# Kernel tuning notes

Hardware: AMD Instinct MI355X
Metric: run time of the kernel (lower is better)

## Reference

```python
import jax, jax.numpy as jnp
import numpy as np

N, DIN, DOUT = 8192, 256, 128
NEG_SLOPE = 0.01         # F.leaky_relu default
MASK_VAL = -9.0e15       # from the torch source


def setup_inputs() -> dict:
    key = jax.random.key(0)
    kx, kadj, kW, kbW, ka1, ka2, kba = jax.random.split(key, 7)
    x = jax.random.normal(kx, (N, DIN), dtype=jnp.float32)
    adj = jax.random.randint(kadj, (N, N), 0, 2, dtype=jnp.int32)
    # Linear W: input_dim -> output_dim
    W = jax.random.normal(kW, (DIN, DOUT), dtype=jnp.float32) * (1.0 / np.sqrt(DIN))
    bW = jax.random.normal(kbW, (DOUT,), dtype=jnp.float32) * 0.01
    # Linear a: 2*output_dim -> 1, split into the h_i part (a1) and h_j part (a2)
    a1 = jax.random.normal(ka1, (DOUT,), dtype=jnp.float32) * (1.0 / np.sqrt(2 * DOUT))
    a2 = jax.random.normal(ka2, (DOUT,), dtype=jnp.float32) * (1.0 / np.sqrt(2 * DOUT))
    ba = jax.random.normal(kba, (), dtype=jnp.float32) * 0.01
    return {"x": x, "adj": adj, "W": W, "bW": bW, "a1": a1, "a2": a2, "ba": ba}


def reference(x, adj, W, bW, a1, a2, ba):
    # h = W x + b  -> [N, DOUT]
    h = x @ W + bW
    # e[i,j] = leaky_relu(a . [h_i, h_j] + ba) = leaky_relu(a1.h_i + a2.h_j + ba)
    s_src = h @ a1            # [N]
    s_dst = h @ a2            # [N]
    e = s_src[:, None] + s_dst[None, :] + ba   # [N, N]
    e = jnp.where(e > 0, e, NEG_SLOPE * e)
    # mask non-edges, row softmax over neighbors j
    e = jnp.where(adj > 0, e, MASK_VAL)
    alpha = jax.nn.softmax(e, axis=1)          # [N, N]
    # dropout is identity in eval mode (dropout_rate=0)
    return alpha @ h                            # [N, DOUT]
```

## Files before the change

### kernel.cpp

```cpp
#include <hip/hip_runtime.h>
#include <hip/hip_bf16.h>


#define NN 8192
#define DIN 256
#define DOUT 128
#define LOG2E 1.4426950408889634f

typedef __attribute__((ext_vector_type(8))) short short8;
typedef __attribute__((ext_vector_type(4))) float floatx4;

__global__ void prep_wt(const float* __restrict__ W, __hip_bfloat16* __restrict__ WT) {
    int e = blockIdx.x * blockDim.x + threadIdx.x;
    if (e < DIN * DOUT) {
        int k = e >> 7;
        int d = e & 127;
        WT[d * DIN + k] = __float2bfloat16(W[e]);
    }
}

__global__ __launch_bounds__(256, 4) void gat_h(
    const float* __restrict__ x, const __hip_bfloat16* __restrict__ WT,
    const float* __restrict__ bW, const float* __restrict__ a1, const float* __restrict__ a2,
    __hip_bfloat16* __restrict__ hbB, float* __restrict__ s_src, float* __restrict__ s_dst) {
    int tid = threadIdx.x;
    int w = tid >> 6, lane = tid & 63;
    int lm = lane & 15, lq = lane >> 4;
    int i0 = blockIdx.x * 32;
    int r0 = (w >> 1) * 16;
    int c0 = (w & 1) * 64;

    __shared__ float s1s[32], s2s[32];
    if (tid < 32) { s1s[tid] = 0.f; s2s[tid] = 0.f; }
    __syncthreads();

    floatx4 acc[4] = {};
#pragma unroll
    for (int kk = 0; kk < DIN; kk += 32) {
        const float4* xp = (const float4*)&x[(size_t)(i0 + r0 + lm) * DIN + kk + lq * 8];
        float4 xa = xp[0], xb = xp[1];
        union { short8 v; __hip_bfloat16 h[8]; } af;
        af.h[0] = __float2bfloat16(xa.x); af.h[1] = __float2bfloat16(xa.y);
        af.h[2] = __float2bfloat16(xa.z); af.h[3] = __float2bfloat16(xa.w);
        af.h[4] = __float2bfloat16(xb.x); af.h[5] = __float2bfloat16(xb.y);
        af.h[6] = __float2bfloat16(xb.z); af.h[7] = __float2bfloat16(xb.w);
#pragma unroll
        for (int t = 0; t < 4; t++) {
            int d = c0 + 16 * t + lm;
            short8 bf = *(const short8*)&WT[(size_t)d * DIN + kk + lq * 8];
            acc[t] = __builtin_amdgcn_mfma_f32_16x16x32_bf16(af.v, bf, acc[t], 0, 0, 0);
        }
    }
    float s1[4] = {0.f, 0.f, 0.f, 0.f}, s2[4] = {0.f, 0.f, 0.f, 0.f};
#pragma unroll
    for (int t = 0; t < 4; t++) {
        int d = c0 + 16 * t + lm;
        int f = (c0 >> 4) + t;
        float A1 = a1[d], A2 = a2[d], B = bW[d];
#pragma unroll
        for (int r = 0; r < 4; r++) {
            int k = r0 + lq * 4 + r;
            float h = acc[t][r] + B;
            hbB[(size_t)blockIdx.x * 4096 + f * 512 + (k >> 3) * 128 + lm * 8 + (k & 7)] =
                __float2bfloat16(h);
            s1[r] += h * A1;
            s2[r] += h * A2;
        }
    }
#pragma unroll
    for (int r = 0; r < 4; r++) {
        for (int m = 1; m < 16; m <<= 1) {
            s1[r] += __shfl_xor(s1[r], m, 64);
            s2[r] += __shfl_xor(s2[r], m, 64);
        }
    }
    if (lm == 0) {
#pragma unroll
        for (int r = 0; r < 4; r++) {
            int row = r0 + lq * 4 + r;
            atomicAdd(&s1s[row], s1[r]);
            atomicAdd(&s2s[row], s2[r]);
        }
    }
    __syncthreads();
    if (tid < 32) {
        s_src[i0 + tid] = s1s[tid] * LOG2E;
        s_dst[i0 + tid] = s2s[tid] * LOG2E;
    }
}

template <int NJT>
__global__ void build_mask(const int* __restrict__ adj, unsigned char* __restrict__ mask) {
    size_t gid = (size_t)blockIdx.x * blockDim.x + threadIdx.x;
    const int4* a = (const int4*)(adj + gid * 8);
    int4 v0 = a[0], v1 = a[1];
    unsigned int b = 0;
    b |= (v0.x != 0) ? 1u : 0u;
    b |= (v0.y != 0) ? 2u : 0u;
    b |= (v0.z != 0) ? 4u : 0u;
    b |= (v0.w != 0) ? 8u : 0u;
    b |= (v1.x != 0) ? 16u : 0u;
    b |= (v1.y != 0) ? 32u : 0u;
    b |= (v1.z != 0) ? 64u : 0u;
    b |= (v1.w != 0) ? 128u : 0u;
    unsigned int g = (unsigned int)gid & (NJT * 4 - 1);
    size_t pos = (gid & ~(size_t)(NJT * 4 - 1)) | ((g & 3) * NJT + (g >> 2));
    mask[pos] = (unsigned char)b;
}

__device__ inline short8 make_pfrag(unsigned int cm, float ssi, float4 cd0, float4 cd1,
                                    floatx4* accd, const short8 ones) {
    float p[8];
    float e;
    e = ssi + cd0.x; e = fmaxf(e, 0.01f * e); p[0] = (cm & 1u)   ? __builtin_amdgcn_exp2f(e) : 0.f;
    e = ssi + cd0.y; e = fmaxf(e, 0.01f * e); p[1] = (cm & 2u)   ? __builtin_amdgcn_exp2f(e) : 0.f;
    e = ssi + cd0.z; e = fmaxf(e, 0.01f * e); p[2] = (cm & 4u)   ? __builtin_amdgcn_exp2f(e) : 0.f;
    e = ssi + cd0.w; e = fmaxf(e, 0.01f * e); p[3] = (cm & 8u)   ? __builtin_amdgcn_exp2f(e) : 0.f;
    e = ssi + cd1.x; e = fmaxf(e, 0.01f * e); p[4] = (cm & 16u)  ? __builtin_amdgcn_exp2f(e) : 0.f;
    e = ssi + cd1.y; e = fmaxf(e, 0.01f * e); p[5] = (cm & 32u)  ? __builtin_amdgcn_exp2f(e) : 0.f;
    e = ssi + cd1.z; e = fmaxf(e, 0.01f * e); p[6] = (cm & 64u)  ? __builtin_amdgcn_exp2f(e) : 0.f;
    e = ssi + cd1.w; e = fmaxf(e, 0.01f * e); p[7] = (cm & 128u) ? __builtin_amdgcn_exp2f(e) : 0.f;
    union { short8 v; __hip_bfloat162 q[4]; } af;
    af.q[0] = __float22bfloat162_rn(make_float2(p[0], p[1]));
    af.q[1] = __float22bfloat162_rn(make_float2(p[2], p[3]));
    af.q[2] = __float22bfloat162_rn(make_float2(p[4], p[5]));
    af.q[3] = __float22bfloat162_rn(make_float2(p[6], p[7]));
    *accd = __builtin_amdgcn_mfma_f32_16x16x32_bf16(af.v, ones, *accd, 0, 0, 0);
    return af.v;
}

template <int NJT>
__global__ __launch_bounds__(256, 3) void gat_attn(
    const unsigned char* __restrict__ mask, const float* __restrict__ s_src,
    const float* __restrict__ s_dst, const float* __restrict__ ba_p,
    const __hip_bfloat16* __restrict__ hbB,
    float* __restrict__ num, float* __restrict__ lpart) {
    int tid = threadIdx.x;
    int w = tid >> 6, lane = tid & 63;
    int lm = lane & 15, lq = lane >> 4;
    int b = blockIdx.x;
    int ib = b & 63;
    int jh = b >> 6;
    int i0 = ib * 128 + w * 32;
    int jb0 = jh * (NJT * 32);

    const unsigned char* mrow0 = mask + (size_t)(i0 + lm) * (NN / 8) + jh * (NJT * 4) + lq * NJT;
    const unsigned char* mrow1 = mrow0 + (size_t)16 * (NN / 8);
    union Mr { uint4 v[NJT / 16]; unsigned int u[NJT / 4]; };
    Mr mr0, mr1;
#pragma unroll
    for (int q = 0; q < NJT / 16; q++) {
        mr0.v[q] = ((const uint4*)mrow0)[q];
        mr1.v[q] = ((const uint4*)mrow1)[q];
    }

    float ba = ba_p[0] * LOG2E;
    float ssi0 = s_src[i0 + lm] + ba;
    float ssi1 = s_src[i0 + 16 + lm] + ba;
    const float* sd = s_dst + jb0 + lq * 8;
    const __hip_bfloat16* hb = hbB + ((size_t)(jh * NJT) * 8) * 512 + lane * 8;

    floatx4 acc0[8] = {}, acc1[8] = {};
    floatx4 accd0 = {}, accd1 = {};
    const short8 ones = { 0x3F80, 0x3F80, 0x3F80, 0x3F80, 0x3F80, 0x3F80, 0x3F80, 0x3F80 };

#pragma unroll
    for (int t = 0; t < NJT; t++) {
        unsigned int cm0 = (mr0.u[t >> 2] >> ((t & 3) * 8)) & 0xFFu;
        unsigned int cm1 = (mr1.u[t >> 2] >> ((t & 3) * 8)) & 0xFFu;
        float4 cd0 = *(const float4*)(sd + t * 32);
        float4 cd1 = *(const float4*)(sd + t * 32 + 4);
        short8 af0 = make_pfrag(cm0, ssi0, cd0, cd1, &accd0, ones);
        short8 af1 = make_pfrag(cm1, ssi1, cd0, cd1, &accd1, ones);

        const __hip_bfloat16* hbt = hb + (size_t)t * 8 * 512;
#pragma unroll
        for (int f = 0; f < 8; f++) {
            short8 bf = *(const short8*)(hbt + f * 512);
            acc0[f] = __builtin_amdgcn_mfma_f32_16x16x32_bf16(af0, bf, acc0[f], 0, 0, 0);
            acc1[f] = __builtin_amdgcn_mfma_f32_16x16x32_bf16(af1, bf, acc1[f], 0, 0, 0);
        }
    }

    float* nb = num + ((size_t)jh * NN + i0) * DOUT;
#pragma unroll
    for (int f = 0; f < 8; f++)
#pragma unroll
        for (int r = 0; r < 4; r++) {
            nb[(size_t)(lq * 4 + r) * DOUT + f * 16 + lm] = acc0[f][r];
            nb[(size_t)(16 + lq * 4 + r) * DOUT + f * 16 + lm] = acc1[f][r];
        }
    if (lm == 0) {
#pragma unroll
        for (int r = 0; r < 4; r++) {
            lpart[(size_t)jh * NN + i0 + lq * 4 + r] = accd0[r];
            lpart[(size_t)jh * NN + i0 + 16 + lq * 4 + r] = accd1[r];
        }
    }
}

__global__ void gat_combine(const float* __restrict__ num, const float* __restrict__ lpart,
                            float* __restrict__ out, int jsplit) {
    int gid = blockIdx.x * blockDim.x + threadIdx.x;
    int idx = gid * 4;
    int i = idx >> 7;
    float den = 0.f;
    for (int s = 0; s < jsplit; s++) den += lpart[(size_t)s * NN + i];
    float inv = 1.0f / den;
    float4 o = make_float4(0.f, 0.f, 0.f, 0.f);
    for (int s = 0; s < jsplit; s++) {
        float4 n = *(const float4*)&num[(size_t)s * NN * DOUT + idx];
        o.x += n.x; o.y += n.y; o.z += n.z; o.w += n.w;
    }
    o.x *= inv; o.y *= inv; o.z *= inv; o.w *= inv;
    *(float4*)&out[idx] = o;
}

extern "C" void kernel_launch(void* const* d_in, const int* in_sizes, int n_in,
                              void* d_out, int out_size, void* d_ws, size_t ws_size,
                              hipStream_t stream) {
    const float* x  = (const float*)d_in[0];
    const int* adj  = (const int*)d_in[1];
    const float* W  = (const float*)d_in[2];
    const float* bW = (const float*)d_in[3];
    const float* a1 = (const float*)d_in[4];
    const float* a2 = (const float*)d_in[5];
    const float* ba = (const float*)d_in[6];
    float* out = (float*)d_out;

    char* ws = (char*)d_ws;
    __hip_bfloat16* hbB  = (__hip_bfloat16*)ws;
    __hip_bfloat16* WT   = (__hip_bfloat16*)(ws + 2097152);
    float* s_src         = (float*)(ws + 2162688);
    float* s_dst         = (float*)(ws + 2195456);
    float* lpart         = (float*)(ws + 2228224);
    unsigned char* mask  = (unsigned char*)(ws + 2752512);
    float* num           = (float*)(ws + 11141120);

    int jsplit = (ws_size >= 11141120 + (size_t)16 * NN * DOUT * 4) ? 16 : 8;

    if (jsplit == 16) build_mask<16><<<32768, 256, 0, stream>>>(adj, mask);
    else              build_mask<32><<<32768, 256, 0, stream>>>(adj, mask);
    prep_wt<<<128, 256, 0, stream>>>(W, WT);
    gat_h<<<256, 256, 0, stream>>>(x, WT, bW, a1, a2, hbB, s_src, s_dst);
    if (jsplit == 16)
        gat_attn<16><<<1024, 256, 0, stream>>>(mask, s_src, s_dst, ba, hbB, num, lpart);
    else
        gat_attn<32><<<512, 256, 0, stream>>>(mask, s_src, s_dst, ba, hbB, num, lpart);
    gat_combine<<<1024, 256, 0, stream>>>(num, lpart, out, jsplit);
}
```

Measured before the change: 440.1 us.

## Fuse adjacency mask building into attention kernel and use nontemporal memory ops

Removes the separate bitmask-packing kernel and has the attention kernel load int32 adjacency values directly with nontemporal loads, testing nonzero per element. This eliminates one full pass over the adjacency matrix plus the packed mask write/read. The attention kernel now streams far more bytes itself, so it may become bandwidth-limited if latency is not hidden. Partial-sum stores and combine loads are also marked nontemporal to reduce cache pollution.

```diff
diff --git a/kernel.cpp b/kernel.cpp
--- a/kernel.cpp
+++ b/kernel.cpp
@@ -9,6 +9,7 @@
 
 typedef __attribute__((ext_vector_type(8))) short short8;
 typedef __attribute__((ext_vector_type(4))) float floatx4;
+typedef __attribute__((ext_vector_type(4))) unsigned int uintx4;
 
 __global__ void prep_wt(const float* __restrict__ W, __hip_bfloat16* __restrict__ WT) {
     int e = blockIdx.x * blockDim.x + threadIdx.x;
@@ -89,37 +90,18 @@
     }
 }
 
-template <int NJT>
-__global__ void build_mask(const int* __restrict__ adj, unsigned char* __restrict__ mask) {
-    size_t gid = (size_t)blockIdx.x * blockDim.x + threadIdx.x;
-    const int4* a = (const int4*)(adj + gid * 8);
-    int4 v0 = a[0], v1 = a[1];
-    unsigned int b = 0;
-    b |= (v0.x != 0) ? 1u : 0u;
-    b |= (v0.y != 0) ? 2u : 0u;
-    b |= (v0.z != 0) ? 4u : 0u;
-    b |= (v0.w != 0) ? 8u : 0u;
-    b |= (v1.x != 0) ? 16u : 0u;
-    b |= (v1.y != 0) ? 32u : 0u;
-    b |= (v1.z != 0) ? 64u : 0u;
-    b |= (v1.w != 0) ? 128u : 0u;
-    unsigned int g = (unsigned int)gid & (NJT * 4 - 1);
-    size_t pos = (gid & ~(size_t)(NJT * 4 - 1)) | ((g & 3) * NJT + (g >> 2));
-    mask[pos] = (unsigned char)b;
-}
-
-__device__ inline short8 make_pfrag(unsigned int cm, float ssi, float4 cd0, float4 cd1,
+__device__ inline short8 make_pfrag(uintx4 m0, uintx4 m1, float ssi, float4 cd0, float4 cd1,
                                     floatx4* accd, const short8 ones) {
     float p[8];
     float e;
-    e = ssi + cd0.x; e = fmaxf(e, 0.01f * e); p[0] = (cm & 1u)   ? __builtin_amdgcn_exp2f(e) : 0.f;
-    e = ssi + cd0.y; e = fmaxf(e, 0.01f * e); p[1] = (cm & 2u)   ? __builtin_amdgcn_exp2f(e) : 0.f;
-    e = ssi + cd0.z; e = fmaxf(e, 0.01f * e); p[2] = (cm & 4u)   ? __builtin_amdgcn_exp2f(e) : 0.f;
-    e = ssi + cd0.w; e = fmaxf(e, 0.01f * e); p[3] = (cm & 8u)   ? __builtin_amdgcn_exp2f(e) : 0.f;
-    e = ssi + cd1.x; e = fmaxf(e, 0.01f * e); p[4] = (cm & 16u)  ? __builtin_amdgcn_exp2f(e) : 0.f;
-    e = ssi + cd1.y; e = fmaxf(e, 0.01f * e); p[5] = (cm & 32u)  ? __builtin_amdgcn_exp2f(e) : 0.f;
-    e = ssi + cd1.z; e = fmaxf(e, 0.01f * e); p[6] = (cm & 64u)  ? __builtin_amdgcn_exp2f(e) : 0.f;
-    e = ssi + cd1.w; e = fmaxf(e, 0.01f * e); p[7] = (cm & 128u) ? __builtin_amdgcn_exp2f(e) : 0.f;
+    e = ssi + cd0.x; e = fmaxf(e, 0.01f * e); p[0] = m0.x ? __builtin_amdgcn_exp2f(e) : 0.f;
+    e = ssi + cd0.y; e = fmaxf(e, 0.01f * e); p[1] = m0.y ? __builtin_amdgcn_exp2f(e) : 0.f;
+    e = ssi + cd0.z; e = fmaxf(e, 0.01f * e); p[2] = m0.z ? __builtin_amdgcn_exp2f(e) : 0.f;
+    e = ssi + cd0.w; e = fmaxf(e, 0.01f * e); p[3] = m0.w ? __builtin_amdgcn_exp2f(e) : 0.f;
+    e = ssi + cd1.x; e = fmaxf(e, 0.01f * e); p[4] = m1.x ? __builtin_amdgcn_exp2f(e) : 0.f;
+    e = ssi + cd1.y; e = fmaxf(e, 0.01f * e); p[5] = m1.y ? __builtin_amdgcn_exp2f(e) : 0.f;
+    e = ssi + cd1.z; e = fmaxf(e, 0.01f * e); p[6] = m1.z ? __builtin_amdgcn_exp2f(e) : 0.f;
+    e = ssi + cd1.w; e = fmaxf(e, 0.01f * e); p[7] = m1.w ? __builtin_amdgcn_exp2f(e) : 0.f;
     union { short8 v; __hip_bfloat162 q[4]; } af;
     af.q[0] = __float22bfloat162_rn(make_float2(p[0], p[1]));
     af.q[1] = __float22bfloat162_rn(make_float2(p[2], p[3]));
@@ -131,7 +113,7 @@
 
 template <int NJT>
 __global__ __launch_bounds__(256, 3) void gat_attn(
-    const unsigned char* __restrict__ mask, const float* __restrict__ s_src,
+    const int* __restrict__ adj, const float* __restrict__ s_src,
     const float* __restrict__ s_dst, const float* __restrict__ ba_p,
     const __hip_bfloat16* __restrict__ hbB,
     float* __restrict__ num, float* __restrict__ lpart) {
@@ -144,15 +126,8 @@
     int i0 = ib * 128 + w * 32;
     int jb0 = jh * (NJT * 32);
 
-    const unsigned char* mrow0 = mask + (size_t)(i0 + lm) * (NN / 8) + jh * (NJT * 4) + lq * NJT;
-    const unsigned char* mrow1 = mrow0 + (size_t)16 * (NN / 8);
-    union Mr { uint4 v[NJT / 16]; unsigned int u[NJT / 4]; };
-    Mr mr0, mr1;
-#pragma unroll
-    for (int q = 0; q < NJT / 16; q++) {
-        mr0.v[q] = ((const uint4*)mrow0)[q];
-        mr1.v[q] = ((const uint4*)mrow1)[q];
-    }
+    const int* arow0 = adj + (size_t)(i0 + lm) * NN + jb0 + lq * 8;
+    const int* arow1 = arow0 + (size_t)16 * NN;
 
     float ba = ba_p[0] * LOG2E;
     float ssi0 = s_src[i0 + lm] + ba;
@@ -166,12 +141,16 @@
 
 #pragma unroll
     for (int t = 0; t < NJT; t++) {
-        unsigned int cm0 = (mr0.u[t >> 2] >> ((t & 3) * 8)) & 0xFFu;
-        unsigned int cm1 = (mr1.u[t >> 2] >> ((t & 3) * 8)) & 0xFFu;
+        const uintx4* a0p = (const uintx4*)(arow0 + t * 32);
+        const uintx4* a1p = (const uintx4*)(arow1 + t * 32);
+        uintx4 m00 = __builtin_nontemporal_load(a0p);
+        uintx4 m01 = __builtin_nontemporal_load(a0p + 1);
+        uintx4 m10 = __builtin_nontemporal_load(a1p);
+        uintx4 m11 = __builtin_nontemporal_load(a1p + 1);
         float4 cd0 = *(const float4*)(sd + t * 32);
         float4 cd1 = *(const float4*)(sd + t * 32 + 4);
-        short8 af0 = make_pfrag(cm0, ssi0, cd0, cd1, &accd0, ones);
-        short8 af1 = make_pfrag(cm1, ssi1, cd0, cd1, &accd1, ones);
+        short8 af0 = make_pfrag(m00, m01, ssi0, cd0, cd1, &accd0, ones);
+        short8 af1 = make_pfrag(m10, m11, ssi1, cd0, cd1, &accd1, ones);
 
         const __hip_bfloat16* hbt = hb + (size_t)t * 8 * 512;
 #pragma unroll
@@ -187,8 +166,10 @@
     for (int f = 0; f < 8; f++)
 #pragma unroll
         for (int r = 0; r < 4; r++) {
-            nb[(size_t)(lq * 4 + r) * DOUT + f * 16 + lm] = acc0[f][r];
-            nb[(size_t)(16 + lq * 4 + r) * DOUT + f * 16 + lm] = acc1[f][r];
+            __builtin_nontemporal_store(acc0[f][r],
+                &nb[(size_t)(lq * 4 + r) * DOUT + f * 16 + lm]);
+            __builtin_nontemporal_store(acc1[f][r],
+                &nb[(size_t)(16 + lq * 4 + r) * DOUT + f * 16 + lm]);
         }
     if (lm == 0) {
 #pragma unroll
@@ -207,13 +188,14 @@
     float den = 0.f;
     for (int s = 0; s < jsplit; s++) den += lpart[(size_t)s * NN + i];
     float inv = 1.0f / den;
-    float4 o = make_float4(0.f, 0.f, 0.f, 0.f);
+    floatx4 o = {0.f, 0.f, 0.f, 0.f};
     for (int s = 0; s < jsplit; s++) {
-        float4 n = *(const float4*)&num[(size_t)s * NN * DOUT + idx];
-        o.x += n.x; o.y += n.y; o.z += n.z; o.w += n.w;
-    }
-    o.x *= inv; o.y *= inv; o.z *= inv; o.w *= inv;
-    *(float4*)&out[idx] = o;
+        floatx4 n = __builtin_nontemporal_load(
+            (const floatx4*)&num[(size_t)s * NN * DOUT + idx]);
+        o += n;
+    }
+    o *= inv;
+    *(floatx4*)&out[idx] = o;
 }
 
 extern "C" void kernel_launch(void* const* d_in, const int* in_sizes, int n_in,
@@ -234,18 +216,15 @@
     float* s_src         = (float*)(ws + 2162688);
     float* s_dst         = (float*)(ws + 2195456);
     float* lpart         = (float*)(ws + 2228224);
-    unsigned char* mask  = (unsigned char*)(ws + 2752512);
-    float* num           = (float*)(ws + 11141120);
-
-    int jsplit = (ws_size >= 11141120 + (size_t)16 * NN * DOUT * 4) ? 16 : 8;
-
-    if (jsplit == 16) build_mask<16><<<32768, 256, 0, stream>>>(adj, mask);
-    else              build_mask<32><<<32768, 256, 0, stream>>>(adj, mask);
+    float* num           = (float*)(ws + 2752512);
+
+    int jsplit = (ws_size >= 2752512 + (size_t)16 * NN * DOUT * 4) ? 16 : 8;
+
     prep_wt<<<128, 256, 0, stream>>>(W, WT);
     gat_h<<<256, 256, 0, stream>>>(x, WT, bW, a1, a2, hbB, s_src, s_dst);
     if (jsplit == 16)
-        gat_attn<16><<<1024, 256, 0, stream>>>(mask, s_src, s_dst, ba, hbB, num, lpart);
+        gat_attn<16><<<1024, 256, 0, stream>>>(adj, s_src, s_dst, ba, hbB, num, lpart);
     else
-        gat_attn<32><<<512, 256, 0, stream>>>(mask, s_src, s_dst, ba, hbB, num, lpart);
+        gat_attn<32><<<512, 256, 0, stream>>>(adj, s_src, s_dst, ba, hbB, num, lpart);
     gat_combine<<<1024, 256, 0, stream>>>(num, lpart, out, jsplit);
 }
```

Measured after the change: 465.7 us. 5.8% more time.

## Process four row groups per wave in attention kernel to reuse h fragments

Applied to the files above, without the earlier changes.

Each wave in the attention kernel now covers 64 rows (four 16-row groups) instead of 32, so every loaded h-fragment feeds four MFMAs instead of two. The grid is halved and launch bounds drop to 2 blocks per CU to make room for the doubled accumulator registers. Partial-result stores and the combine kernel's loads are switched to nontemporal accesses to limit cache pollution. Higher register use lowers occupancy, and with only 512 or 256 blocks the GPU may have fewer waves for latency hiding.

```diff
diff --git a/kernel.cpp b/kernel.cpp
--- a/kernel.cpp
+++ b/kernel.cpp
@@ -130,7 +130,7 @@
 }
 
 template <int NJT>
-__global__ __launch_bounds__(256, 3) void gat_attn(
+__global__ __launch_bounds__(256, 2) void gat_attn(
     const unsigned char* __restrict__ mask, const float* __restrict__ s_src,
     const float* __restrict__ s_dst, const float* __restrict__ ba_p,
     const __hip_bfloat16* __restrict__ hbB,
@@ -139,63 +139,66 @@
     int w = tid >> 6, lane = tid & 63;
     int lm = lane & 15, lq = lane >> 4;
     int b = blockIdx.x;
-    int ib = b & 63;
-    int jh = b >> 6;
-    int i0 = ib * 128 + w * 32;
+    int ib = b & 31;
+    int jh = b >> 5;
+    int i0 = ib * 256 + w * 64;
     int jb0 = jh * (NJT * 32);
 
-    const unsigned char* mrow0 = mask + (size_t)(i0 + lm) * (NN / 8) + jh * (NJT * 4) + lq * NJT;
-    const unsigned char* mrow1 = mrow0 + (size_t)16 * (NN / 8);
     union Mr { uint4 v[NJT / 16]; unsigned int u[NJT / 4]; };
-    Mr mr0, mr1;
-#pragma unroll
-    for (int q = 0; q < NJT / 16; q++) {
-        mr0.v[q] = ((const uint4*)mrow0)[q];
-        mr1.v[q] = ((const uint4*)mrow1)[q];
-    }
+    Mr mr[4];
+    const unsigned char* mrow = mask + (size_t)(i0 + lm) * (NN / 8) + jh * (NJT * 4) + lq * NJT;
+#pragma unroll
+    for (int rg = 0; rg < 4; rg++)
+#pragma unroll
+        for (int q = 0; q < NJT / 16; q++)
+            mr[rg].v[q] = ((const uint4*)(mrow + (size_t)rg * 16 * (NN / 8)))[q];
 
     float ba = ba_p[0] * LOG2E;
-    float ssi0 = s_src[i0 + lm] + ba;
-    float ssi1 = s_src[i0 + 16 + lm] + ba;
+    float ssi[4];
+#pragma unroll
+    for (int rg = 0; rg < 4; rg++) ssi[rg] = s_src[i0 + rg * 16 + lm] + ba;
     const float* sd = s_dst + jb0 + lq * 8;
     const __hip_bfloat16* hb = hbB + ((size_t)(jh * NJT) * 8) * 512 + lane * 8;
 
-    floatx4 acc0[8] = {}, acc1[8] = {};
-    floatx4 accd0 = {}, accd1 = {};
+    floatx4 acc[4][8] = {};
+    floatx4 accd[4] = {};
     const short8 ones = { 0x3F80, 0x3F80, 0x3F80, 0x3F80, 0x3F80, 0x3F80, 0x3F80, 0x3F80 };
 
 #pragma unroll
     for (int t = 0; t < NJT; t++) {
-        unsigned int cm0 = (mr0.u[t >> 2] >> ((t & 3) * 8)) & 0xFFu;
-        unsigned int cm1 = (mr1.u[t >> 2] >> ((t & 3) * 8)) & 0xFFu;
         float4 cd0 = *(const float4*)(sd + t * 32);
         float4 cd1 = *(const float4*)(sd + t * 32 + 4);
-        short8 af0 = make_pfrag(cm0, ssi0, cd0, cd1, &accd0, ones);
-        short8 af1 = make_pfrag(cm1, ssi1, cd0, cd1, &accd1, ones);
-
+        short8 af[4];
+#pragma unroll
+        for (int rg = 0; rg < 4; rg++) {
+            unsigned int cm = (mr[rg].u[t >> 2] >> ((t & 3) * 8)) & 0xFFu;
+            af[rg] = make_pfrag(cm, ssi[rg], cd0, cd1, &accd[rg], ones);
+        }
         const __hip_bfloat16* hbt = hb + (size_t)t * 8 * 512;
 #pragma unroll
         for (int f = 0; f < 8; f++) {
             short8 bf = *(const short8*)(hbt + f * 512);
-            acc0[f] = __builtin_amdgcn_mfma_f32_16x16x32_bf16(af0, bf, acc0[f], 0, 0, 0);
-            acc1[f] = __builtin_amdgcn_mfma_f32_16x16x32_bf16(af1, bf, acc1[f], 0, 0, 0);
+#pragma unroll
+            for (int rg = 0; rg < 4; rg++)
+                acc[rg][f] = __builtin_amdgcn_mfma_f32_16x16x32_bf16(af[rg], bf, acc[rg][f], 0, 0, 0);
         }
     }
 
     float* nb = num + ((size_t)jh * NN + i0) * DOUT;
 #pragma unroll
-    for (int f = 0; f < 8; f++)
-#pragma unroll
-        for (int r = 0; r < 4; r++) {
-            nb[(size_t)(lq * 4 + r) * DOUT + f * 16 + lm] = acc0[f][r];
-            nb[(size_t)(16 + lq * 4 + r) * DOUT + f * 16 + lm] = acc1[f][r];
-        }
+    for (int rg = 0; rg < 4; rg++)
+#pragma unroll
+        for (int f = 0; f < 8; f++)
+#pragma unroll
+            for (int r = 0; r < 4; r++)
+                __builtin_nontemporal_store(acc[rg][f][r],
+                    &nb[(size_t)(rg * 16 + lq * 4 + r) * DOUT + f * 16 + lm]);
     if (lm == 0) {
 #pragma unroll
-        for (int r = 0; r < 4; r++) {
-            lpart[(size_t)jh * NN + i0 + lq * 4 + r] = accd0[r];
-            lpart[(size_t)jh * NN + i0 + 16 + lq * 4 + r] = accd1[r];
-        }
+        for (int rg = 0; rg < 4; rg++)
+#pragma unroll
+            for (int r = 0; r < 4; r++)
+                lpart[(size_t)jh * NN + i0 + rg * 16 + lq * 4 + r] = accd[rg][r];
     }
 }
 
@@ -207,13 +210,14 @@
     float den = 0.f;
     for (int s = 0; s < jsplit; s++) den += lpart[(size_t)s * NN + i];
     float inv = 1.0f / den;
-    float4 o = make_float4(0.f, 0.f, 0.f, 0.f);
+    floatx4 o = {0.f, 0.f, 0.f, 0.f};
     for (int s = 0; s < jsplit; s++) {
-        float4 n = *(const float4*)&num[(size_t)s * NN * DOUT + idx];
-        o.x += n.x; o.y += n.y; o.z += n.z; o.w += n.w;
-    }
-    o.x *= inv; o.y *= inv; o.z *= inv; o.w *= inv;
-    *(float4*)&out[idx] = o;
+        floatx4 n = __builtin_nontemporal_load(
+            (const floatx4*)&num[(size_t)s * NN * DOUT + idx]);
+        o += n;
+    }
+    o *= inv;
+    *(floatx4*)&out[idx] = o;
 }
 
 extern "C" void kernel_launch(void* const* d_in, const int* in_sizes, int n_in,
@@ -244,8 +248,8 @@
     prep_wt<<<128, 256, 0, stream>>>(W, WT);
     gat_h<<<256, 256, 0, stream>>>(x, WT, bW, a1, a2, hbB, s_src, s_dst);
     if (jsplit == 16)
-        gat_attn<16><<<1024, 256, 0, stream>>>(mask, s_src, s_dst, ba, hbB, num, lpart);
+        gat_attn<16><<<512, 256, 0, stream>>>(mask, s_src, s_dst, ba, hbB, num, lpart);
     else
-        gat_attn<32><<<512, 256, 0, stream>>>(mask, s_src, s_dst, ba, hbB, num, lpart);
+        gat_attn<32><<<256, 256, 0, stream>>>(mask, s_src, s_dst, ba, hbB, num, lpart);
     gat_combine<<<1024, 256, 0, stream>>>(num, lpart, out, jsplit);
 }
```

New measurement: 434.7 us. About the same (-1.2%).
